# Optimization experiments

Hardware: AMD Instinct MI355X
Metric: run time of the kernel (lower is better)

## Reference

```python
import jax, jax.numpy as jnp
import numpy as np

BATCH, C_IN, C_OUT, N_GRID, N_MODES = 64, 64, 64, 8192, 64
SCALE = 1.0 / (C_IN * C_OUT)


def setup_inputs() -> dict:
    key = jax.random.key(0)
    k1, k2, k3 = jax.random.split(key, 3)
    lhss = jax.random.normal(k1, (BATCH, C_IN, N_GRID), dtype=jnp.float32)
    # torch.rand on cfloat draws real and imag uniformly in [0,1), then scaled
    w_real = SCALE * jax.random.uniform(k2, (C_IN, C_OUT, N_MODES), dtype=jnp.float32)
    w_imag = SCALE * jax.random.uniform(k3, (C_IN, C_OUT, N_MODES), dtype=jnp.float32)
    return {"lhss": lhss, "w_real": w_real, "w_imag": w_imag}


def reference(lhss, w_real, w_imag):
    n = lhss.shape[-1]
    n_freq = n // 2 + 1  # rfft output length
    weights = w_real + 1j * w_imag  # (c_in, c_out, modes), complex64
    xf = jnp.fft.rfft(lhss)  # (b, c_in, n_freq) complex
    # complex channel-mixing on the first N_MODES frequency bins only
    mixed = jnp.einsum("bix,iox->box", xf[:, :, :N_MODES], weights)
    # zero-pad remaining high-frequency bins, then inverse rfft
    res = jnp.zeros((lhss.shape[0], weights.shape[1], n_freq), dtype=mixed.dtype)
    res = res.at[:, :, :N_MODES].set(mixed)
    return jnp.fft.irfft(res, n=n)
```

## Files before the change

kernel.cpp:

```cpp
#include <hip/hip_runtime.h>
#include <hip/hip_bf16.h>

#define NG 8192
#define NB 64
#define CI 64
#define CO 64
#define NM 64
#define NFJ 128
#define NROWS 4096

typedef __bf16 bf16x8 __attribute__((ext_vector_type(8)));
typedef float f32x4 __attribute__((ext_vector_type(4)));

#define GLOAD_LDS16(gsrc, ldst)                                                   \
    __builtin_amdgcn_global_load_lds(                                             \
        (const __attribute__((address_space(1))) void*)(gsrc),                    \
        (__attribute__((address_space(3))) void*)(ldst), 16, 0, 0)


__global__ __launch_bounds__(256) void sc_prep(const float* __restrict__ wr,
                                               const float* __restrict__ wi,
                                               __bf16* __restrict__ Ft,
                                               __bf16* __restrict__ Ginv,
                                               __bf16* __restrict__ Wtf) {
    __shared__ __align__(16) __bf16 wlds[16384];
    const float W0 = 6.2831853071795864769f / (float)NG;
    if (blockIdx.x >= 64) {
        int idx = (blockIdx.x - 64) * 256 + threadIdx.x;
        if (idx < 128 * NG) {
            int j = idx >> 13, pos = idx & (NG - 1);
            int blk = pos >> 6, g = (pos >> 3) & 7, e = pos & 7;
            int ksrc = (blk << 6) + (((g ^ (j & 7)) << 3) | e);
            int m = j >> 1;
            int t = (m * ksrc) & (NG - 1);
            float s, c;
            __sincosf((float)t * W0, &s, &c);
            Ft[idx] = (__bf16)((j & 1) ? -s : c);
        } else {
            int i2 = idx - 128 * NG;
            int n = i2 >> 7, pos = i2 & 127;
            int g = pos >> 3, e = pos & 7;
            int psrc = ((g ^ (n & 15)) << 3) | e;
            int m = psrc >> 1, im = psrc & 1;
            int t = (m * n) & (NG - 1);
            float s, c;
            __sincosf((float)t * W0, &s, &c);
            float v;
            if (im) v = (m == 0) ? 0.0f : (-2.0f / NG) * s;
            else    v = ((m == 0) ? 1.0f : 2.0f) / NG * c;
            Ginv[i2] = (__bf16)v;
        }
    } else {
        const int m = blockIdx.x;
        const int t = threadIdx.x;
        const int o = t & 63, q = t >> 6;
        const int ot = o >> 4, l = o & 15;
        float wrv[16], wiv[16];
        #pragma unroll
        for (int cc = 0; cc < 16; ++cc) {
            int ci = q * 16 + cc;
            wrv[cc] = wr[((size_t)ci * 64 + o) * 64 + m];
            wiv[cc] = wi[((size_t)ci * 64 + o) * 64 + m];
        }
        #pragma unroll
        for (int cc = 0; cc < 16; ++cc) {
            int ci = q * 16 + cc;
            int ksa = ci >> 5, ksb = 2 + ksa;
            int kg = (ci >> 3) & 3, e = ci & 7;
            int pos = (kg * 16 + l) * 8 + e;
            wlds[(0*16 + ksa*4 + ot)*512 + pos] = (__bf16)wrv[cc];
            wlds[(0*16 + ksb*4 + ot)*512 + pos] = (__bf16)(-wiv[cc]);
            wlds[(1*16 + ksa*4 + ot)*512 + pos] = (__bf16)wiv[cc];
            wlds[(1*16 + ksb*4 + ot)*512 + pos] = (__bf16)wrv[cc];
        }
        __syncthreads();
        const uint4* src = (const uint4*)wlds;
        uint4* dst = (uint4*)(Wtf + (size_t)m * 16384);
        #pragma unroll
        for (int s = 0; s < 8; ++s)
            dst[s * 256 + t] = src[s * 256 + t];
    }
}

__global__ __launch_bounds__(256) void sc_dft(const float* __restrict__ A,
                                              const __bf16* __restrict__ Ft,
                                              float* __restrict__ XFp,
                                              int nsteps) {
    __shared__ __align__(16) char smem[49152];
    char* A0 = smem;
    char* A1 = smem + 8192;
    char* F0 = smem + 16384;
    char* F1 = smem + 32768;

    const int tid = threadIdx.x;
    const int w = tid >> 6, lane = tid & 63;
    const int l15 = lane & 15, kg = lane >> 4;
    const int wm = w >> 1, wn = w & 1;
    const int rt = blockIdx.x & 63, sp = blockIdx.x >> 6;
    const int r0 = rt * 64;
    const size_t kb0 = (size_t)sp * nsteps * 64;
    const int swz = l15 & 7;

    float4 av[4];
    f32x4 acc[2][4] = {};

    auto issueA = [&](int step) {
        size_t kb = kb0 + (size_t)step * 64;
        #pragma unroll
        for (int s = 0; s < 4; ++s) {
            int c = s * 256 + tid;
            av[s] = *(const float4*)(A + (size_t)(r0 + (c >> 4)) * NG + kb + (c & 15) * 4);
        }
    };
    auto writeA = [&](char* Ab) {
        #pragma unroll
        for (int s = 0; s < 4; ++s) {
            int c = s * 256 + tid, row = c >> 4, cq = c & 15;
            union { __bf16 h[4]; uint2 u; } cv;
            cv.h[0] = (__bf16)av[s].x; cv.h[1] = (__bf16)av[s].y;
            cv.h[2] = (__bf16)av[s].z; cv.h[3] = (__bf16)av[s].w;
            *(uint2*)(Ab + row * 128 + (((cq >> 1) ^ (row & 7)) << 4) + ((cq & 1) << 3)) = cv.u;
        }
    };
    auto stageF = [&](int step, char* Fb) {
        size_t kb = kb0 + (size_t)step * 64;
        #pragma unroll
        for (int s = 0; s < 4; ++s) {
            int cc = s * 256 + tid;
            GLOAD_LDS16(Ft + (size_t)(cc >> 3) * NG + kb + (cc & 7) * 8, Fb + cc * 16);
        }
    };
    auto compute = [&](const char* Ab, const char* Fb) {
        #pragma unroll
        for (int ks2 = 0; ks2 < 2; ++ks2) {
            bf16x8 a[2], b[4];
            #pragma unroll
            for (int mt = 0; mt < 2; ++mt)
                a[mt] = *(const bf16x8*)(Ab + (wm*32 + mt*16 + l15) * 128 +
                                         (((ks2*4 + kg) ^ swz) << 4));
            #pragma unroll
            for (int jt = 0; jt < 4; ++jt)
                b[jt] = *(const bf16x8*)(Fb + (wn*64 + jt*16 + l15) * 128 +
                                         (((ks2*4 + kg) ^ swz) << 4));
            #pragma unroll
            for (int mt = 0; mt < 2; ++mt)
                #pragma unroll
                for (int jt = 0; jt < 4; ++jt)
                    acc[mt][jt] = __builtin_amdgcn_mfma_f32_16x16x32_bf16(
                        a[mt], b[jt], acc[mt][jt], 0, 0, 0);
        }
    };

    issueA(0); stageF(0, F0); writeA(A0);
    __syncthreads();
    for (int t = 0; t < nsteps; ++t) {
        char* Ac = (t & 1) ? A1 : A0;
        char* Fc = (t & 1) ? F1 : F0;
        char* An = (t & 1) ? A0 : A1;
        char* Fn = (t & 1) ? F0 : F1;
        if (t + 1 < nsteps) { issueA(t + 1); stageF(t + 1, Fn); }
        compute(Ac, Fc);
        if (t + 1 < nsteps) writeA(An);
        __syncthreads();
    }
    #pragma unroll
    for (int mt = 0; mt < 2; ++mt)
        #pragma unroll
        for (int jt = 0; jt < 4; ++jt)
            *(f32x4*)(XFp + ((size_t)sp * NFJ + wn*64 + jt*16 + l15) * NROWS +
                      (r0 + wm*32 + mt*16 + kg*4)) = acc[mt][jt];
}

__global__ __launch_bounds__(256) void sc_mix(const float* __restrict__ XFp,
                                              const __bf16* __restrict__ Wtf,
                                              __bf16* __restrict__ M2, int nsplit) {
    __shared__ __align__(16) char at[4096];
    const int t = threadIdx.x;
    const int k = blockIdx.x >> 2, bq = blockIdx.x & 3;
    const int lane = t & 63, ot = t >> 6;
    const int l15 = lane & 15, kg = lane >> 4;

    const int c = t >> 7, t127 = t & 127;
    f32x4 s0 = {}, s1 = {};
    {
        const float* src = XFp + (size_t)(2*k + c) * NROWS + bq*1024 + t127*8;
        const size_t pstride = (size_t)NFJ * NROWS;
        if (nsplit == 8) {
            #pragma unroll
            for (int p = 0; p < 8; ++p) {
                s0 += *(const f32x4*)(src + p*pstride);
                s1 += *(const f32x4*)(src + p*pstride + 4);
            }
        } else {
            for (int p = 0; p < nsplit; ++p) {
                s0 += *(const f32x4*)(src + p*pstride);
                s1 += *(const f32x4*)(src + p*pstride + 4);
            }
        }
    }
    {
        const int bl = t127 >> 3;
        const int i0 = (t127 & 7) * 8;
        union { __bf16 h[8]; uint4 u; } cv;
        cv.h[0]=(__bf16)s0[0]; cv.h[1]=(__bf16)s0[1];
        cv.h[2]=(__bf16)s0[2]; cv.h[3]=(__bf16)s0[3];
        cv.h[4]=(__bf16)s1[0]; cv.h[5]=(__bf16)s1[1];
        cv.h[6]=(__bf16)s1[2]; cv.h[7]=(__bf16)s1[3];
        *(uint4*)(at + bl*256 + ((((c*64 + i0) >> 3) ^ bl) << 4)) = cv.u;
    }
    __syncthreads();

    bf16x8 a[4];
    #pragma unroll
    for (int ks = 0; ks < 4; ++ks)
        a[ks] = *(const bf16x8*)(at + l15*256 + (((ks*4 + kg) ^ l15) << 4));

    f32x4 accR = {}, accI = {};
    #pragma unroll
    for (int ks = 0; ks < 4; ++ks) {
        bf16x8 b0 = *(const bf16x8*)(Wtf + (size_t)(((k*2+0)*4+ks)*4+ot)*512 + lane*8);
        accR = __builtin_amdgcn_mfma_f32_16x16x32_bf16(a[ks], b0, accR, 0, 0, 0);
    }
    #pragma unroll
    for (int ks = 0; ks < 4; ++ks) {
        bf16x8 b1 = *(const bf16x8*)(Wtf + (size_t)(((k*2+1)*4+ks)*4+ot)*512 + lane*8);
        accI = __builtin_amdgcn_mfma_f32_16x16x32_bf16(a[ks], b1, accI, 0, 0, 0);
    }
    #pragma unroll
    for (int rr = 0; rr < 4; ++rr) {
        int bg = bq*16 + kg*4 + rr;
        size_t r = (size_t)bg * CO + ot*16 + l15;
        ushort2 pk;
        pk.x = __builtin_bit_cast(unsigned short, (__bf16)accR[rr]);
        pk.y = __builtin_bit_cast(unsigned short, (__bf16)accI[rr]);
        *(ushort2*)(M2 + r * NFJ + 2 * k) = pk;
    }
}

__global__ __launch_bounds__(512) void sc_idft(const __bf16* __restrict__ M2,
                                               const __bf16* __restrict__ Ginv,
                                               float* __restrict__ out) {
    __shared__ __align__(16) char gls[32768];
    const int tid = threadIdx.x;
    const int w = tid >> 6, lane = tid & 63;
    const int l15 = lane & 15, kg = lane >> 4;
    const int wm = w >> 1;
    const int wn = w & 1;
    const int r0 = (blockIdx.x >> 6) * 128;
    const int n0 = (blockIdx.x & 63) * 128;

    #pragma unroll
    for (int s = 0; s < 4; ++s) {
        int cc = s * 512 + tid;
        GLOAD_LDS16(Ginv + (size_t)n0 * NFJ + cc * 8, gls + cc * 16);
    }

    bf16x8 af[2][4];
    #pragma unroll
    for (int mt = 0; mt < 2; ++mt)
        #pragma unroll
        for (int ks = 0; ks < 4; ++ks)
            af[mt][ks] = *(const bf16x8*)(M2 + (size_t)(r0 + wm*32 + mt*16 + l15) * NFJ +
                                          ks*32 + kg*8);
    __syncthreads();

    f32x4 acc[2][4] = {};
    #pragma unroll
    for (int nt = 0; nt < 4; ++nt) {
        int row = wn*64 + nt*16 + l15;
        bf16x8 bfr[4];
        #pragma unroll
        for (int ks = 0; ks < 4; ++ks)
            bfr[ks] = *(const bf16x8*)(gls + row * 256 + (((ks*4 + kg) ^ (row & 15)) << 4));
        #pragma unroll
        for (int mt = 0; mt < 2; ++mt)
            #pragma unroll
            for (int ks = 0; ks < 4; ++ks)
                acc[mt][nt] = __builtin_amdgcn_mfma_f32_16x16x32_bf16(
                    bfr[ks], af[mt][ks], acc[mt][nt], 0, 0, 0);
    }
    #pragma unroll
    for (int mt = 0; mt < 2; ++mt)
        #pragma unroll
        for (int nt = 0; nt < 4; ++nt)
            *(f32x4*)(out + (size_t)(r0 + wm*32 + mt*16 + l15) * NG +
                      n0 + wn*64 + nt*16 + kg*4) = acc[mt][nt];
}

extern "C" void kernel_launch(void* const* d_in, const int* in_sizes, int n_in,
                              void* d_out, int out_size, void* d_ws, size_t ws_size,
                              hipStream_t stream) {
    const float* lhss = (const float*)d_in[0];
    const float* w_real = (const float*)d_in[1];
    const float* w_imag = (const float*)d_in[2];
    float* out = (float*)d_out;

    char* ws = (char*)d_ws;
    __bf16* Ft_sw   = (__bf16*)ws;
    __bf16* Ginv_sw = (__bf16*)(ws + (2u << 20));
    __bf16* M2      = (__bf16*)(ws + (6u << 20));
    __bf16* Wtf     = (__bf16*)(ws + (7u << 20));
    float*  XFp     = (float*) (ws + (9u << 20));

    int split;
    if      (ws_size >= (25u << 20)) split = 8;
    else if (ws_size >= (17u << 20)) split = 4;
    else if (ws_size >= (13u << 20)) split = 2;
    else                             split = 1;
    int nsteps = 128 / split;

    sc_prep<<<8256, 256, 0, stream>>>(w_real, w_imag, Ft_sw, Ginv_sw, Wtf);
    sc_dft<<<64 * split, 256, 0, stream>>>(lhss, Ft_sw, XFp, nsteps);
    sc_mix<<<256, 256, 0, stream>>>(XFp, Wtf, M2, split);
    sc_idft<<<2048, 512, 0, stream>>>(M2, Ginv_sw, out);
}
```

Before: 96.45 us.

## Load DFT GEMM operands directly from global memory into registers, drop LDS staging

The forward-DFT GEMM kernel no longer stages the input rows and the twiddle matrix through double-buffered shared memory. Each lane now loads its MFMA fragments straight from global memory, converting fp32 to bf16 in registers. The twiddle table is stored unswizzled to match. This removes LDS traffic and block-wide barriers, but it drops cross-wave reuse: each row of A is now read by both wn waves, each F row by both wm waves, and loads are only 32-byte segments per lane.

```diff
diff --git a/kernel.cpp b/kernel.cpp
--- a/kernel.cpp
+++ b/kernel.cpp
@@ -28,11 +28,9 @@
     if (blockIdx.x >= 64) {
         int idx = (blockIdx.x - 64) * 256 + threadIdx.x;
         if (idx < 128 * NG) {
-            int j = idx >> 13, pos = idx & (NG - 1);
-            int blk = pos >> 6, g = (pos >> 3) & 7, e = pos & 7;
-            int ksrc = (blk << 6) + (((g ^ (j & 7)) << 3) | e);
+            int j = idx >> 13, k = idx & (NG - 1);
             int m = j >> 1;
-            int t = (m * ksrc) & (NG - 1);
+            int t = (m * k) & (NG - 1);
             float s, c;
             __sincosf((float)t * W0, &s, &c);
             Ft[idx] = (__bf16)((j & 1) ? -s : c);
@@ -82,87 +80,59 @@
     }
 }
 
-__global__ __launch_bounds__(256) void sc_dft(const float* __restrict__ A,
-                                              const __bf16* __restrict__ Ft,
-                                              float* __restrict__ XFp,
-                                              int nsteps) {
-    __shared__ __align__(16) char smem[49152];
-    char* A0 = smem;
-    char* A1 = smem + 8192;
-    char* F0 = smem + 16384;
-    char* F1 = smem + 32768;
-
+__global__ __launch_bounds__(256, 2) void sc_dft(const float* __restrict__ A,
+                                                 const __bf16* __restrict__ Ft,
+                                                 float* __restrict__ XFp,
+                                                 int nsteps) {
     const int tid = threadIdx.x;
     const int w = tid >> 6, lane = tid & 63;
     const int l15 = lane & 15, kg = lane >> 4;
     const int wm = w >> 1, wn = w & 1;
     const int rt = blockIdx.x & 63, sp = blockIdx.x >> 6;
     const int r0 = rt * 64;
-    const size_t kb0 = (size_t)sp * nsteps * 64;
-    const int swz = l15 & 7;
-
-    float4 av[4];
+    const int ksl = nsteps * 64;
+    const size_t kb0 = (size_t)sp * ksl;
+
+    const float*  a0p = A  + (size_t)(r0 + wm*32 + l15) * NG + kb0 + kg*8;
+    const float*  a1p = a0p + (size_t)16 * NG;
+    const __bf16* bp  = Ft + (size_t)(wn*64 + l15) * NG + kb0 + kg*8;
+
     f32x4 acc[2][4] = {};
 
-    auto issueA = [&](int step) {
-        size_t kb = kb0 + (size_t)step * 64;
-        #pragma unroll
-        for (int s = 0; s < 4; ++s) {
-            int c = s * 256 + tid;
-            av[s] = *(const float4*)(A + (size_t)(r0 + (c >> 4)) * NG + kb + (c & 15) * 4);
-        }
-    };
-    auto writeA = [&](char* Ab) {
-        #pragma unroll
-        for (int s = 0; s < 4; ++s) {
-            int c = s * 256 + tid, row = c >> 4, cq = c & 15;
-            union { __bf16 h[4]; uint2 u; } cv;
-            cv.h[0] = (__bf16)av[s].x; cv.h[1] = (__bf16)av[s].y;
-            cv.h[2] = (__bf16)av[s].z; cv.h[3] = (__bf16)av[s].w;
-            *(uint2*)(Ab + row * 128 + (((cq >> 1) ^ (row & 7)) << 4) + ((cq & 1) << 3)) = cv.u;
-        }
-    };
-    auto stageF = [&](int step, char* Fb) {
-        size_t kb = kb0 + (size_t)step * 64;
-        #pragma unroll
-        for (int s = 0; s < 4; ++s) {
-            int cc = s * 256 + tid;
-            GLOAD_LDS16(Ft + (size_t)(cc >> 3) * NG + kb + (cc & 7) * 8, Fb + cc * 16);
-        }
-    };
-    auto compute = [&](const char* Ab, const char* Fb) {
-        #pragma unroll
-        for (int ks2 = 0; ks2 < 2; ++ks2) {
-            bf16x8 a[2], b[4];
-            #pragma unroll
-            for (int mt = 0; mt < 2; ++mt)
-                a[mt] = *(const bf16x8*)(Ab + (wm*32 + mt*16 + l15) * 128 +
-                                         (((ks2*4 + kg) ^ swz) << 4));
+    #pragma unroll 2
+    for (int kk = 0; kk < ksl; kk += 32) {
+        bf16x8 a[2], b[4];
+        {
+            float4 lo = *(const float4*)(a0p + kk);
+            float4 hi = *(const float4*)(a0p + kk + 4);
+            union { __bf16 h[8]; bf16x8 v; } cv;
+            cv.h[0]=(__bf16)lo.x; cv.h[1]=(__bf16)lo.y;
+            cv.h[2]=(__bf16)lo.z; cv.h[3]=(__bf16)lo.w;
+            cv.h[4]=(__bf16)hi.x; cv.h[5]=(__bf16)hi.y;
+            cv.h[6]=(__bf16)hi.z; cv.h[7]=(__bf16)hi.w;
+            a[0] = cv.v;
+        }
+        {
+            float4 lo = *(const float4*)(a1p + kk);
+            float4 hi = *(const float4*)(a1p + kk + 4);
+            union { __bf16 h[8]; bf16x8 v; } cv;
+            cv.h[0]=(__bf16)lo.x; cv.h[1]=(__bf16)lo.y;
+            cv.h[2]=(__bf16)lo.z; cv.h[3]=(__bf16)lo.w;
+            cv.h[4]=(__bf16)hi.x; cv.h[5]=(__bf16)hi.y;
+            cv.h[6]=(__bf16)hi.z; cv.h[7]=(__bf16)hi.w;
+            a[1] = cv.v;
+        }
+        #pragma unroll
+        for (int jt = 0; jt < 4; ++jt)
+            b[jt] = *(const bf16x8*)(bp + (size_t)jt * 16 * NG + kk);
+        #pragma unroll
+        for (int mt = 0; mt < 2; ++mt)
             #pragma unroll
             for (int jt = 0; jt < 4; ++jt)
-                b[jt] = *(const bf16x8*)(Fb + (wn*64 + jt*16 + l15) * 128 +
-                                         (((ks2*4 + kg) ^ swz) << 4));
-            #pragma unroll
-            for (int mt = 0; mt < 2; ++mt)
-                #pragma unroll
-                for (int jt = 0; jt < 4; ++jt)
-                    acc[mt][jt] = __builtin_amdgcn_mfma_f32_16x16x32_bf16(
-                        a[mt], b[jt], acc[mt][jt], 0, 0, 0);
-        }
-    };
-
-    issueA(0); stageF(0, F0); writeA(A0);
-    __syncthreads();
-    for (int t = 0; t < nsteps; ++t) {
-        char* Ac = (t & 1) ? A1 : A0;
-        char* Fc = (t & 1) ? F1 : F0;
-        char* An = (t & 1) ? A0 : A1;
-        char* Fn = (t & 1) ? F0 : F1;
-        if (t + 1 < nsteps) { issueA(t + 1); stageF(t + 1, Fn); }
-        compute(Ac, Fc);
-        if (t + 1 < nsteps) writeA(An);
-        __syncthreads();
-    }
+                acc[mt][jt] = __builtin_amdgcn_mfma_f32_16x16x32_bf16(
+                    a[mt], b[jt], acc[mt][jt], 0, 0, 0);
+    }
+
     #pragma unroll
     for (int mt = 0; mt < 2; ++mt)
         #pragma unroll
@@ -296,7 +266,7 @@
     float* out = (float*)d_out;
 
     char* ws = (char*)d_ws;
-    __bf16* Ft_sw   = (__bf16*)ws;
+    __bf16* Ft      = (__bf16*)ws;
     __bf16* Ginv_sw = (__bf16*)(ws + (2u << 20));
     __bf16* M2      = (__bf16*)(ws + (6u << 20));
     __bf16* Wtf     = (__bf16*)(ws + (7u << 20));
@@ -309,8 +279,8 @@
     else                             split = 1;
     int nsteps = 128 / split;
 
-    sc_prep<<<8256, 256, 0, stream>>>(w_real, w_imag, Ft_sw, Ginv_sw, Wtf);
-    sc_dft<<<64 * split, 256, 0, stream>>>(lhss, Ft_sw, XFp, nsteps);
+    sc_prep<<<8256, 256, 0, stream>>>(w_real, w_imag, Ft, Ginv_sw, Wtf);
+    sc_dft<<<64 * split, 256, 0, stream>>>(lhss, Ft, XFp, nsteps);
     sc_mix<<<256, 256, 0, stream>>>(XFp, Wtf, M2, split);
     sc_idft<<<2048, 512, 0, stream>>>(M2, Ginv_sw, out);
 }
```

Result: slower. 137.6 us (+42.7%).

## Deepen DFT GEMM pipeline with two-step-ahead A prefetch and manual waitcnt barriers

Applied to the files above, without the earlier changes.

The A tile loads in the DFT GEMM kernel now use two register buffers, so global loads are issued two steps ahead instead of one. __syncthreads is replaced by explicit s_waitcnt with a partial vmcnt and s_barrier, which lets the newer A loads stay in flight across the barrier. Launch bounds add a minimum of 2 blocks per CU. The cost is more registers and hand-managed wait counts that rely on the order in which loads are issued.

```diff
diff --git a/kernel.cpp b/kernel.cpp
--- a/kernel.cpp
+++ b/kernel.cpp
@@ -82,15 +82,15 @@
     }
 }
 
-__global__ __launch_bounds__(256) void sc_dft(const float* __restrict__ A,
-                                              const __bf16* __restrict__ Ft,
-                                              float* __restrict__ XFp,
-                                              int nsteps) {
+__global__ __launch_bounds__(256, 2) void sc_dft(const float* __restrict__ A,
+                                                 const __bf16* __restrict__ Ft,
+                                                 float* __restrict__ XFp,
+                                                 int nsteps) {
     __shared__ __align__(16) char smem[49152];
-    char* A0 = smem;
-    char* A1 = smem + 8192;
-    char* F0 = smem + 16384;
-    char* F1 = smem + 32768;
+    char* Ab0 = smem;
+    char* Ab1 = smem + 8192;
+    char* Fb0 = smem + 16384;
+    char* Fb1 = smem + 32768;
 
     const int tid = threadIdx.x;
     const int w = tid >> 6, lane = tid & 63;
@@ -101,10 +101,10 @@
     const size_t kb0 = (size_t)sp * nsteps * 64;
     const int swz = l15 & 7;
 
-    float4 av[4];
+    float4 avA[4], avB[4];
     f32x4 acc[2][4] = {};
 
-    auto issueA = [&](int step) {
+    auto issueA = [&](int step, float4 (&av)[4]) {
         size_t kb = kb0 + (size_t)step * 64;
         #pragma unroll
         for (int s = 0; s < 4; ++s) {
@@ -112,7 +112,7 @@
             av[s] = *(const float4*)(A + (size_t)(r0 + (c >> 4)) * NG + kb + (c & 15) * 4);
         }
     };
-    auto writeA = [&](char* Ab) {
+    auto writeA = [&](const float4 (&av)[4], char* Ab) {
         #pragma unroll
         for (int s = 0; s < 4; ++s) {
             int c = s * 256 + tid, row = c >> 4, cq = c & 15;
@@ -151,18 +151,37 @@
         }
     };
 
-    issueA(0); stageF(0, F0); writeA(A0);
-    __syncthreads();
+    stageF(0, Fb0);
+    __builtin_amdgcn_sched_barrier(0);
+    issueA(0, avA);
+    writeA(avA, Ab0);
+    issueA(1, avB);
+    asm volatile("s_waitcnt lgkmcnt(0)" ::: "memory");
+    __builtin_amdgcn_s_barrier();
+    __builtin_amdgcn_sched_barrier(0);
+
     for (int t = 0; t < nsteps; ++t) {
-        char* Ac = (t & 1) ? A1 : A0;
-        char* Fc = (t & 1) ? F1 : F0;
-        char* An = (t & 1) ? A0 : A1;
-        char* Fn = (t & 1) ? F0 : F1;
-        if (t + 1 < nsteps) { issueA(t + 1); stageF(t + 1, Fn); }
+        const bool evn = !(t & 1);
+        const char* Ac = evn ? Ab0 : Ab1;
+        const char* Fc = evn ? Fb0 : Fb1;
+        char* An = evn ? Ab1 : Ab0;
+        char* Fn = evn ? Fb1 : Fb0;
+        if (t + 1 < nsteps) stageF(t + 1, Fn);
+        __builtin_amdgcn_sched_barrier(0);
+        if (t + 2 < nsteps) { if (evn) issueA(t + 2, avA); else issueA(t + 2, avB); }
         compute(Ac, Fc);
-        if (t + 1 < nsteps) writeA(An);
-        __syncthreads();
-    }
+        if (t + 1 < nsteps) {
+            if (evn) writeA(avB, An); else writeA(avA, An);
+            if (t + 2 < nsteps)
+                asm volatile("s_waitcnt vmcnt(4)" ::: "memory");
+            else
+                asm volatile("s_waitcnt vmcnt(0)" ::: "memory");
+            asm volatile("s_waitcnt lgkmcnt(0)" ::: "memory");
+            __builtin_amdgcn_s_barrier();
+            __builtin_amdgcn_sched_barrier(0);
+        }
+    }
+
     #pragma unroll
     for (int mt = 0; mt < 2; ++mt)
         #pragma unroll
```

After: 97.83 us. Within noise of the previous version (+1.4%).
